# Kernel tuning notes

Hardware: AMD Instinct MI355X
Metric: run time of the kernel (lower is better)

Reference implementation:

```python
import jax, jax.numpy as jnp
import numpy as np

B, C, N = 8, 128, 4096
OUT = 256
K = 16
BN_EPS = 1e-5


def setup_inputs() -> dict:
    key = jax.random.key(0)
    k1, k2, k3 = jax.random.split(key, 3)
    x = jax.random.normal(k1, (B, C, N), dtype=jnp.float32)
    # Conv1d with kernel_size=1 is a pointwise linear: weight (OUT, C)
    conv_w = jax.random.normal(k2, (OUT, C), dtype=jnp.float32) * (1.0 / np.sqrt(C))
    conv_b = jax.random.normal(k3, (OUT,), dtype=jnp.float32) * 0.01
    bn_gamma = jnp.ones((OUT,), dtype=jnp.float32)
    bn_beta = jnp.zeros((OUT,), dtype=jnp.float32)
    return {"x": x, "conv_w": conv_w, "conv_b": conv_b,
            "bn_gamma": bn_gamma, "bn_beta": bn_beta, "k": K}


def reference(x, conv_w, conv_b, bn_gamma, bn_beta, k):
    # x: (B, C, N)
    xt = jnp.swapaxes(x, 1, 2)                    # (B, N, C)
    sq = jnp.sum(xt * xt, axis=-1)                # (B, N)
    inner = jnp.einsum('bnc,bmc->bnm', xt, xt)    # (B, N, N)
    # pairwise = -||xi - xj||^2
    pairwise = 2.0 * inner - sq[:, :, None] - sq[:, None, :]
    _, idx = jax.lax.top_k(pairwise, k)           # (B, N, k), k nearest (incl. self)

    # gather neighbor features: (B, N, k, C)
    knn_x = jax.vmap(lambda pts, i: pts[i])(xt, idx)
    pooled = jnp.max(knn_x, axis=2)               # (B, N, C)

    # pointwise conv (kernel size 1)
    y = jnp.einsum('bnc,oc->bno', pooled, conv_w) + conv_b  # (B, N, OUT)

    # BatchNorm1d in training mode: batch stats over (B, N) per channel
    mean = jnp.mean(y, axis=(0, 1))
    var = jnp.mean((y - mean) ** 2, axis=(0, 1))  # biased variance
    y = (y - mean) * jax.lax.rsqrt(var + BN_EPS) * bn_gamma + bn_beta
    y = jax.nn.relu(y)
    return jnp.swapaxes(y, 1, 2)                  # (B, OUT, N)
```

## Files before the change

### kernel.cpp

```cpp
#include <hip/hip_runtime.h>
#include <cfloat>
#include <climits>
#include <cstdint>

#define B_ 8
#define C_ 128
#define N_ 4096
#define OUT_ 256
#define K_ 16
#define NC_ 24
#define BN_ (B_ * N_)
#define SBIAS 200.0f

typedef __attribute__((ext_vector_type(8))) short s16x8;
typedef __attribute__((ext_vector_type(16))) float f32x16;

static __device__ __forceinline__ ushort f2bf(float f) {
  uint32_t u = __float_as_uint(f);
  uint32_t r = (u + 0x7fffu + ((u >> 16) & 1u)) >> 16;
  return (ushort)r;
}
static __device__ __forceinline__ float bf2f(ushort u) {
  return __uint_as_float(((uint32_t)u) << 16);
}

__global__ __launch_bounds__(256) void k_sq_xt(const float* __restrict__ x,
                                               float* __restrict__ sq,
                                               float* __restrict__ xt,
                                               ushort* __restrict__ xb16) {
  const int b = blockIdx.x >> 6;
  const int n0 = (blockIdx.x & 63) << 6;
  __shared__ float xs[C_][65];
  const float* xb = x + (size_t)b * C_ * N_;
  for (int id = threadIdx.x; id < C_ * 64; id += 256) {
    const int c = id >> 6, n = id & 63;
    xs[c][n] = xb[(size_t)c * N_ + n0 + n];
  }
  __syncthreads();
  if (threadIdx.x < 64) {
    const int n = threadIdx.x;
    float acc = 0.f;
#pragma unroll
    for (int c = 0; c < C_; ++c) { const float v = xs[c][n]; acc = fmaf(v, v, acc); }
    sq[b * N_ + n0 + n] = acc;
  }
  const int r = threadIdx.x >> 2;
  const int p = threadIdx.x & 3;
  float* dst = xt + ((size_t)(b * N_ + n0 + r)) * C_ + p * 32;
#pragma unroll
  for (int c0 = 0; c0 < 32; c0 += 4) {
    float4 o;
    o.x = xs[p * 32 + c0 + 0][r];
    o.y = xs[p * 32 + c0 + 1][r];
    o.z = xs[p * 32 + c0 + 2][r];
    o.w = xs[p * 32 + c0 + 3][r];
    *(float4*)(dst + c0) = o;
  }
  ushort* bdst = xb16 + ((size_t)(b * N_ + n0 + r)) * C_ + p * 32;
#pragma unroll
  for (int c0 = 0; c0 < 32; c0 += 8) {
    s16x8 o;
#pragma unroll
    for (int e = 0; e < 8; ++e) o[e] = (short)f2bf(xs[p * 32 + c0 + e][r]);
    *(s16x8*)(bdst + c0) = o;
  }
}

__global__ __launch_bounds__(256) void k_wprep(const float* __restrict__ w,
                                               ushort* __restrict__ wb16) {
  const int i = blockIdx.x * 256 + threadIdx.x;
  wb16[i] = f2bf(w[i]);
}

__global__ __launch_bounds__(256, 2) void k_knn_mfma(
    const ushort* __restrict__ xb16, const float* __restrict__ sq,
    int* __restrict__ cand) {
  const int b  = blockIdx.x >> 6;
  const int i0 = (blockIdx.x & 63) << 6;
  const int t  = threadIdx.x;
  const int w  = t >> 6;
  const int lane = t & 63;
  const int g = w >> 1;
  const int h = w & 1;

  __shared__ unsigned lds_lists[64 * 64];

  const ushort* xbB = xb16 + (((size_t)b) << 12) * C_;
  const float* sqB = sq + (b << 12);
  const int ibase = i0 + (g << 5);
  const int jh0 = h << 11;

  s16x8 bfr[8];
  {
    const ushort* ip = xbB + ((size_t)(ibase + (lane & 31))) * C_ + (lane >> 5) * 8;
#pragma unroll
    for (int ks = 0; ks < 8; ++ks) bfr[ks] = *(const s16x8*)(ip + ks * 16);
  }

  unsigned lst[K_];
#pragma unroll
  for (int m = 0; m < K_; ++m) lst[m] = 0u;

  const ushort* aplane = xbB + (size_t)(lane & 31) * C_ + (lane >> 5) * 8;
  const float* sqlane = sqB + 4 * (lane >> 5);
  const unsigned vb2 = 4095u - 4u * (unsigned)(lane >> 5);

  s16x8 afA[8], afB[8];
  float4 sqA[4], sqB4[4];

#define LOADT(AF, SQ, J0)                                                  \
  {                                                                        \
    const ushort* ap = aplane + (size_t)(J0) * C_;                         \
    _Pragma("unroll")                                                      \
    for (int ks = 0; ks < 8; ++ks) (AF)[ks] = *(const s16x8*)(ap + ks * 16); \
    _Pragma("unroll")                                                      \
    for (int u = 0; u < 4; ++u) (SQ)[u] = *(const float4*)(sqlane + (J0) + 8 * u); \
  }

#define COMPT(AF, SQ, J0)                                                  \
  {                                                                        \
    f32x16 acc;                                                            \
    _Pragma("unroll")                                                      \
    for (int r = 0; r < 16; ++r) {                                         \
      const float sv = (r & 1) ? ((r & 2) ? (SQ)[r >> 2].w : (SQ)[r >> 2].y) \
                               : ((r & 2) ? (SQ)[r >> 2].z : (SQ)[r >> 2].x); \
      acc[r] = fmaf(sv, -0.5f, SBIAS);                                     \
    }                                                                      \
    acc = __builtin_amdgcn_mfma_f32_32x32x16_bf16((AF)[0], bfr[0], acc, 0, 0, 0); \
    _Pragma("unroll")                                                      \
    for (int ks = 1; ks < 8; ++ks)                                         \
      acc = __builtin_amdgcn_mfma_f32_32x32x16_bf16((AF)[ks], bfr[ks], acc, 0, 0, 0); \
    _Pragma("unroll")                                                      \
    for (int r = 0; r < 16; ++r) {                                         \
      const unsigned u = __float_as_uint(acc[r]);                          \
      unsigned p = (u & 0xFFFFF000u) | (vb2 - (unsigned)((J0) + (r & 3) + 8 * (r >> 2))); \
      _Pragma("unroll")                                                    \
      for (int m = 0; m < K_; ++m) {                                       \
        const unsigned mx = p > lst[m] ? p : lst[m];                       \
        const unsigned mn = p > lst[m] ? lst[m] : p;                       \
        lst[m] = mx; p = mn;                                               \
      }                                                                    \
    }                                                                      \
  }

  LOADT(afA, sqA, jh0);
  for (int jt = 0; jt < 64; jt += 2) {
    const int j0e = jh0 + jt * 32;
    LOADT(afB, sqB4, j0e + 32);
    COMPT(afA, sqA, j0e);
    if (jt + 2 < 64) LOADT(afA, sqA, j0e + 64);
    COMPT(afB, sqB4, j0e + 32);
  }

  {
    const int rl = (g << 5) + (lane & 31);
    const int listid = (h << 1) + (lane >> 5);
    unsigned* dst = &lds_lists[(rl * 4 + listid) * 16];
#pragma unroll
    for (int m = 0; m < K_; ++m) dst[m] = lst[m];
  }
  __syncthreads();

  const int up = lane >> 5;
  const int ladj = up ? (lane ^ 31) : lane;
  const int run = lane >> 4;
  const int slot = (run & 1) ? (15 - (lane & 15)) : (lane & 15);
  for (int rr = 0; rr < 16; ++rr) {
    const int row = (w << 4) + rr;
    unsigned v = lds_lists[row * 64 + run * 16 + slot];
#pragma unroll
    for (int ms = 16; ms >= 1; ms >>= 1) {
      const unsigned pv = __shfl_xor(v, ms, 64);
      const unsigned mx = v > pv ? v : pv;
      const unsigned mn = v > pv ? pv : v;
      v = ((ladj & ms) == 0) ? mx : mn;
    }
#pragma unroll
    for (int ms = 32; ms >= 1; ms >>= 1) {
      const unsigned pv = __shfl_xor(v, ms, 64);
      const unsigned mx = v > pv ? v : pv;
      const unsigned mn = v > pv ? pv : v;
      v = ((lane & ms) == 0) ? mx : mn;
    }
    if (lane < NC_) {
      const int j = 4095 - (int)(v & 0xFFFu);
      cand[((size_t)((b << 12) + i0 + row)) * NC_ + lane] = j;
    }
  }
}

__global__ __launch_bounds__(256) void k_refine_gather(
    const float* __restrict__ xt, const int* __restrict__ cand,
    ushort* __restrict__ pooled16) {
  const int half = threadIdx.x >> 5;
  const int l = threadIdx.x & 31;
  const int row = blockIdx.x * 8 + half;
  const int b = row >> 12;
  const size_t bbase = (size_t)(b << 12);
  const float4* xr4 = (const float4*)(xt + (size_t)row * C_);
  double d = DBL_MAX;
  int j = INT_MAX;
  if (l < NC_) {
    j = cand[(size_t)row * NC_ + l];
    const float4* xj4 = (const float4*)(xt + (bbase + j) * C_);
    double acc = 0.0;
#pragma unroll 8
    for (int c = 0; c < C_ / 4; ++c) {
      const float4 a = xr4[c];
      const float4 v = xj4[c];
      const double dx = (double)a.x - (double)v.x;
      const double dy = (double)a.y - (double)v.y;
      const double dz = (double)a.z - (double)v.z;
      const double dw = (double)a.w - (double)v.w;
      acc += dx * dx + dy * dy + dz * dz + dw * dw;
    }
    d = acc;
  }
  int win[K_];
#pragma unroll
  for (int m = 0; m < K_; ++m) {
    double bd = d; int bj = j;
#pragma unroll
    for (int off = 16; off > 0; off >>= 1) {
      const double od = __shfl_xor(bd, off, 32);
      const int oj = __shfl_xor(bj, off, 32);
      if (od < bd || (od == bd && oj < bj)) { bd = od; bj = oj; }
    }
    win[m] = bj;
    if (bj == j) d = DBL_MAX;
  }
  const int c0 = l * 4;
  float4 mx = make_float4(-FLT_MAX, -FLT_MAX, -FLT_MAX, -FLT_MAX);
#pragma unroll
  for (int m = 0; m < K_; ++m) {
    const float4 v = *(const float4*)(xt + (bbase + win[m]) * C_ + c0);
    mx.x = fmaxf(mx.x, v.x);
    mx.y = fmaxf(mx.y, v.y);
    mx.z = fmaxf(mx.z, v.z);
    mx.w = fmaxf(mx.w, v.w);
  }
  ushort4 o;
  o.x = f2bf(mx.x); o.y = f2bf(mx.y); o.z = f2bf(mx.z); o.w = f2bf(mx.w);
  *(ushort4*)(pooled16 + (size_t)row * C_ + c0) = o;
}

__global__ __launch_bounds__(256) void k_conv_y(const ushort* __restrict__ pooled16,
                                                const ushort* __restrict__ wb16,
                                                const float* __restrict__ bias,
                                                ushort* __restrict__ y16) {
  const int i0 = blockIdx.x << 7;
  const int b = i0 >> 12;
  const int nb = i0 & (N_ - 1);
  const int t = threadIdx.x, w = t >> 6, l = t & 63;
  __shared__ float biasl[OUT_];
  biasl[t] = bias[t];
  __syncthreads();
  const int kh = l >> 5;
  const int irow = i0 + (w << 5) + (l & 31);
  s16x8 pf[8];
  {
    const ushort* pp = pooled16 + (size_t)irow * C_ + kh * 8;
#pragma unroll
    for (int ks = 0; ks < 8; ++ks) pf[ks] = *(const s16x8*)(pp + ks * 16);
  }
  const int nout = nb + (w << 5) + (l & 31);
  for (int ot = 0; ot < 8; ++ot) {
    const ushort* wp = wb16 + (size_t)(ot * 32 + (l & 31)) * C_ + kh * 8;
    s16x8 wf[8];
#pragma unroll
    for (int ks = 0; ks < 8; ++ks) wf[ks] = *(const s16x8*)(wp + ks * 16);
    f32x16 acc;
#pragma unroll
    for (int r = 0; r < 16; ++r) acc[r] = 0.f;
#pragma unroll
    for (int ks = 0; ks < 8; ++ks)
      acc = __builtin_amdgcn_mfma_f32_32x32x16_bf16(wf[ks], pf[ks], acc, 0, 0, 0);
#pragma unroll
    for (int r = 0; r < 16; ++r) {
      const int o = ot * 32 + (r & 3) + 8 * (r >> 2) + 4 * kh;
      const float y = acc[r] + biasl[o];
      y16[((size_t)(b * OUT_ + o) << 12) + nout] = f2bf(y);
    }
  }
}

__global__ __launch_bounds__(256) void k_ystats(const ushort* __restrict__ y16,
                                                const float* __restrict__ gamma,
                                                const float* __restrict__ beta,
                                                float2* __restrict__ ss) {
  const int o = blockIdx.x;
  const int t = threadIdx.x;
  float s1 = 0.f, s2 = 0.f;
  for (int b = 0; b < B_; ++b) {
    const ushort* yp = y16 + ((size_t)(b * OUT_ + o) << 12);
#pragma unroll
    for (int it = 0; it < 2; ++it) {
      const s16x8 v = *(const s16x8*)(yp + (it * 256 + t) * 8);
#pragma unroll
      for (int e = 0; e < 8; ++e) {
        const float f = bf2f((ushort)v[e]);
        s1 += f;
        s2 = fmaf(f, f, s2);
      }
    }
  }
#pragma unroll
  for (int off = 32; off > 0; off >>= 1) {
    s1 += __shfl_xor(s1, off, 64);
    s2 += __shfl_xor(s2, off, 64);
  }
  __shared__ float r1[4], r2[4];
  if ((t & 63) == 0) { r1[t >> 6] = s1; r2[t >> 6] = s2; }
  __syncthreads();
  if (t == 0) {
    const float S1 = r1[0] + r1[1] + r1[2] + r1[3];
    const float S2 = r2[0] + r2[1] + r2[2] + r2[3];
    const float inv = 1.f / (float)BN_;
    const float mean = S1 * inv;
    const float var = S2 * inv - mean * mean;
    const float scale = gamma[o] / sqrtf(var + 1e-5f);
    float2 r; r.x = scale; r.y = beta[o] - mean * scale;
    ss[o] = r;
  }
}

__global__ __launch_bounds__(256) void k_bn(const ushort* __restrict__ y16,
                                            const float2* __restrict__ ss,
                                            float* __restrict__ out) {
  const size_t idx = ((size_t)blockIdx.x * 256 + threadIdx.x) * 4;
  const int o = (int)((idx >> 12) & (OUT_ - 1));
  const float2 sv = ss[o];
  const ushort4 v = *(const ushort4*)(y16 + idx);
  float4 r;
  r.x = fmaxf(fmaf(bf2f(v.x), sv.x, sv.y), 0.f);
  r.y = fmaxf(fmaf(bf2f(v.y), sv.x, sv.y), 0.f);
  r.z = fmaxf(fmaf(bf2f(v.z), sv.x, sv.y), 0.f);
  r.w = fmaxf(fmaf(bf2f(v.w), sv.x, sv.y), 0.f);
  *(float4*)(out + idx) = r;
}

extern "C" void kernel_launch(void* const* d_in, const int* in_sizes, int n_in,
                              void* d_out, int out_size, void* d_ws, size_t ws_size,
                              hipStream_t stream) {
  const float* x      = (const float*)d_in[0];
  const float* conv_w = (const float*)d_in[1];
  const float* conv_b = (const float*)d_in[2];
  const float* gamma  = (const float*)d_in[3];
  const float* beta   = (const float*)d_in[4];
  float* out = (float*)d_out;

  float* ws = (float*)d_ws;
  float* sq = ws;
  float* xt = sq + BN_;
  ushort* y16 = (ushort*)xt;
  int*   cand = (int*)(xt + (size_t)BN_ * C_);
  ushort* pooled16 = (ushort*)(cand + (size_t)BN_ * NC_);
  ushort* xb16 = pooled16 + (size_t)BN_ * C_;
  ushort* wb16 = xb16 + (size_t)BN_ * C_;
  float2* ss = (float2*)(wb16 + (size_t)OUT_ * C_);

  k_sq_xt<<<B_ * (N_ / 64), 256, 0, stream>>>(x, sq, xt, xb16);
  k_wprep<<<(OUT_ * C_) / 256, 256, 0, stream>>>(conv_w, wb16);
  k_knn_mfma<<<B_ * (N_ / 64), 256, 0, stream>>>(xb16, sq, cand);
  k_refine_gather<<<BN_ / 8, 256, 0, stream>>>(xt, cand, pooled16);
  k_conv_y<<<BN_ / 128, 256, 0, stream>>>(pooled16, wb16, conv_b, y16);
  k_ystats<<<OUT_, 256, 0, stream>>>(y16, gamma, beta, ss);
  k_bn<<<(BN_ * OUT_ / 4) / 256, 256, 0, stream>>>(y16, ss, out);
}
```

Baseline: 348.3 us.

## Split kNN column range across four waves per 32-row tile and merge eight lists

The kNN kernel now handles 32 query rows per block, with each of the four waves scanning a quarter of the candidate columns, instead of two row groups times two column halves. Twice as many blocks are launched, and launch bounds ask for 4 blocks per CU to raise occupancy. The final merge now bitonic-sorts two 64-entry runs per row and combines them, where it previously sorted one. This adds shuffle work in the merge, and each block reloads the column tiles for fewer rows, which doubles global/L2 traffic for the A operand.

```diff
diff --git a/kernel.cpp b/kernel.cpp
--- a/kernel.cpp
+++ b/kernel.cpp
@@ -72,27 +72,25 @@
   wb16[i] = f2bf(w[i]);
 }
 
-__global__ __launch_bounds__(256, 2) void k_knn_mfma(
+__global__ __launch_bounds__(256, 4) void k_knn_mfma(
     const ushort* __restrict__ xb16, const float* __restrict__ sq,
     int* __restrict__ cand) {
-  const int b  = blockIdx.x >> 6;
-  const int i0 = (blockIdx.x & 63) << 6;
+  const int b  = blockIdx.x >> 7;
+  const int i0 = (blockIdx.x & 127) << 5;
   const int t  = threadIdx.x;
   const int w  = t >> 6;
   const int lane = t & 63;
-  const int g = w >> 1;
-  const int h = w & 1;
-
-  __shared__ unsigned lds_lists[64 * 64];
+  const int kh = lane >> 5;
+
+  __shared__ unsigned lds_lists[32 * 128];
 
   const ushort* xbB = xb16 + (((size_t)b) << 12) * C_;
   const float* sqB = sq + (b << 12);
-  const int ibase = i0 + (g << 5);
-  const int jh0 = h << 11;
+  const int jq0 = w << 10;
 
   s16x8 bfr[8];
   {
-    const ushort* ip = xbB + ((size_t)(ibase + (lane & 31))) * C_ + (lane >> 5) * 8;
+    const ushort* ip = xbB + ((size_t)(i0 + (lane & 31))) * C_ + (lane >> 5) * 8;
 #pragma unroll
     for (int ks = 0; ks < 8; ++ks) bfr[ks] = *(const s16x8*)(ip + ks * 16);
   }
@@ -143,19 +141,19 @@
     }                                                                      \
   }
 
-  LOADT(afA, sqA, jh0);
-  for (int jt = 0; jt < 64; jt += 2) {
-    const int j0e = jh0 + jt * 32;
+  LOADT(afA, sqA, jq0);
+  for (int jt = 0; jt < 32; jt += 2) {
+    const int j0e = jq0 + jt * 32;
     LOADT(afB, sqB4, j0e + 32);
     COMPT(afA, sqA, j0e);
-    if (jt + 2 < 64) LOADT(afA, sqA, j0e + 64);
+    if (jt + 2 < 32) LOADT(afA, sqA, j0e + 64);
     COMPT(afB, sqB4, j0e + 32);
   }
 
   {
-    const int rl = (g << 5) + (lane & 31);
-    const int listid = (h << 1) + (lane >> 5);
-    unsigned* dst = &lds_lists[(rl * 4 + listid) * 16];
+    const int rl = lane & 31;
+    const int listid = (w << 1) + kh;
+    unsigned* dst = &lds_lists[(rl * 8 + listid) * 16];
 #pragma unroll
     for (int m = 0; m < K_; ++m) dst[m] = lst[m];
   }
@@ -165,16 +163,40 @@
   const int ladj = up ? (lane ^ 31) : lane;
   const int run = lane >> 4;
   const int slot = (run & 1) ? (15 - (lane & 15)) : (lane & 15);
-  for (int rr = 0; rr < 16; ++rr) {
-    const int row = (w << 4) + rr;
-    unsigned v = lds_lists[row * 64 + run * 16 + slot];
+  for (int rr = 0; rr < 8; ++rr) {
+    const int row = (w << 3) + rr;
+    const unsigned* base = &lds_lists[row * 128];
+    unsigned vA = base[run * 16 + slot];
+    unsigned vB = base[64 + run * 16 + slot];
 #pragma unroll
     for (int ms = 16; ms >= 1; ms >>= 1) {
-      const unsigned pv = __shfl_xor(v, ms, 64);
-      const unsigned mx = v > pv ? v : pv;
-      const unsigned mn = v > pv ? pv : v;
-      v = ((ladj & ms) == 0) ? mx : mn;
-    }
+      const unsigned pv = __shfl_xor(vA, ms, 64);
+      const unsigned mx = vA > pv ? vA : pv;
+      const unsigned mn = vA > pv ? pv : vA;
+      vA = ((ladj & ms) == 0) ? mx : mn;
+    }
+#pragma unroll
+    for (int ms = 32; ms >= 1; ms >>= 1) {
+      const unsigned pv = __shfl_xor(vA, ms, 64);
+      const unsigned mx = vA > pv ? vA : pv;
+      const unsigned mn = vA > pv ? pv : vA;
+      vA = ((lane & ms) == 0) ? mx : mn;
+    }
+#pragma unroll
+    for (int ms = 16; ms >= 1; ms >>= 1) {
+      const unsigned pv = __shfl_xor(vB, ms, 64);
+      const unsigned mx = vB > pv ? vB : pv;
+      const unsigned mn = vB > pv ? pv : vB;
+      vB = ((ladj & ms) == 0) ? mx : mn;
+    }
+#pragma unroll
+    for (int ms = 32; ms >= 1; ms >>= 1) {
+      const unsigned pv = __shfl_xor(vB, ms, 64);
+      const unsigned mx = vB > pv ? vB : pv;
+      const unsigned mn = vB > pv ? pv : vB;
+      vB = ((lane & ms) != 0) ? mx : mn;
+    }
+    unsigned v = vA > vB ? vA : vB;
 #pragma unroll
     for (int ms = 32; ms >= 1; ms >>= 1) {
       const unsigned pv = __shfl_xor(v, ms, 64);
@@ -361,7 +383,7 @@
 
   k_sq_xt<<<B_ * (N_ / 64), 256, 0, stream>>>(x, sq, xt, xb16);
   k_wprep<<<(OUT_ * C_) / 256, 256, 0, stream>>>(conv_w, wb16);
-  k_knn_mfma<<<B_ * (N_ / 64), 256, 0, stream>>>(xb16, sq, cand);
+  k_knn_mfma<<<B_ * (N_ / 32), 256, 0, stream>>>(xb16, sq, cand);
   k_refine_gather<<<BN_ / 8, 256, 0, stream>>>(xt, cand, pooled16);
   k_conv_y<<<BN_ / 128, 256, 0, stream>>>(pooled16, wb16, conv_b, y16);
   k_ystats<<<OUT_, 256, 0, stream>>>(y16, gamma, beta, ss);
```

After: 484.6 us. 1.39x slower.
